# Kernel tuning notes

Hardware: AMD Instinct MI355X
Metric: run time of the kernel (lower is better)

The kernel has to match this reference:

```python
import jax, jax.numpy as jnp
import numpy as np


def setup_inputs() -> dict:
    key = jax.random.key(0)
    k1, k2, k3 = jax.random.split(key, 3)
    B, S, D, H = 16, 4096, 512, 512
    inp = jax.random.normal(k1, (B, S, D), dtype=jnp.float32)
    # torch nn.Linear(D, 3*H): weight (3H, D), bias (3H,)
    W = jax.random.normal(k2, (3 * H, D), dtype=jnp.float32) * (1.0 / np.sqrt(D))
    b = jax.random.normal(k3, (3 * H,), dtype=jnp.float32) * 0.01
    return {"inp": inp, "W": W, "b": b}


def _forget_mult(z, f):
    # z, f: (B, S, H). h_t = f_t*z_t + (1-f_t)*h_{t-1}, h_{-1}=0 (hid=None)
    zt = jnp.swapaxes(z, 0, 1)  # (S, B, H)
    ft = jnp.swapaxes(f, 0, 1)
    h0 = jnp.zeros(z.shape[0:1] + z.shape[2:3], dtype=z.dtype)  # (B, H)

    def step(h, zf):
        zi, fi = zf
        h = fi * zi + (1.0 - fi) * h
        return h, h

    _, hs = jax.lax.scan(step, h0, (zt, ft))
    return jnp.swapaxes(hs, 0, 1)  # (B, S, H)


def reference(inp, W, b):
    # QRNNLayer forward: window=1, output_gate=True, batch_first=True,
    # backward=False, zoneout=0, hid=None.
    y = jnp.einsum('bsd,hd->bsh', inp, W) + b  # (B, S, 3H)
    z_gate, f_gate, o_gate = jnp.split(y, 3, axis=2)
    z_gate = jnp.tanh(z_gate)
    f_gate = jax.nn.sigmoid(f_gate)
    c_gate = _forget_mult(z_gate, f_gate)
    output = jax.nn.sigmoid(o_gate) * c_gate
    return output, c_gate[:, -1]
```

## Files before the change

### kernel.cpp

```cpp
#include <hip/hip_runtime.h>
#include <stdint.h>

#define Bdim 16
#define Sdim 4096
#define Hdim 512
#define Mdim (Bdim*Sdim)
#define N3   (3*Hdim)
#define Kdim 512
#define NCHUNK 128
#define CLEN  (Sdim/NCHUNK)

typedef __bf16 bf16;
typedef __bf16 bf16x4 __attribute__((ext_vector_type(4)));
typedef __bf16 bf16x8 __attribute__((ext_vector_type(8)));
typedef float  f32x4  __attribute__((ext_vector_type(4)));
typedef _Float16 f16;
typedef _Float16 f16x8 __attribute__((ext_vector_type(8)));

__device__ __forceinline__ void gload_lds16(const void* g, void* l) {
  __builtin_amdgcn_global_load_lds(
      (const __attribute__((address_space(1))) uint32_t*)g,
      (__attribute__((address_space(3))) uint32_t*)l, 16, 0, 0);
}

__global__ void __launch_bounds__(256) cvt2_kernel(const float4* __restrict__ a,
                                                   bf16x4* __restrict__ oa, int nA,
                                                   const float4* __restrict__ w,
                                                   bf16x4* __restrict__ ow, int nW) {
  int i = blockIdx.x * blockDim.x + threadIdx.x;
  const float4* src; bf16x4* dst; int j;
  if (i < nA) { src = a; dst = oa; j = i; }
  else { j = i - nA; if (j >= nW) return; src = w; dst = ow; }
  float4 v = src[j];
  bf16x4 o;
  o.x = (bf16)v.x; o.y = (bf16)v.y; o.z = (bf16)v.z; o.w = (bf16)v.w;
  dst[j] = o;
}

#define BM 128
#define BN 256
#define BK2 32
#define NT (Kdim/BK2)
#define LBUF 24576

__global__ void __launch_bounds__(512, 4) gemm_act_kernel(
    const bf16* __restrict__ A, const bf16* __restrict__ Wb,
    const float* __restrict__ bias,
    f16* __restrict__ zbuf, f16* __restrict__ fbuf, f16* __restrict__ ogbuf) {
  __shared__ char lds[2 * LBUF];
  const int tid  = threadIdx.x;
  const int wid  = tid >> 6;
  const int lane = tid & 63;
  const int wr = wid >> 2, wc = wid & 3;
  const int bid = blockIdx.x;
  const int wg  = (bid & 7) * 384 + (bid >> 3);
  const int mt = wg / (N3 / BN);
  const int nt = wg % (N3 / BN);
  const int row0 = mt * BM;

  const bf16* Ag = A  + (size_t)row0 * Kdim;
  const bf16* Bg = Wb + (size_t)(nt * BN) * Kdim;

  uint32_t srcA;
  {
    int row = tid >> 2, slot = tid & 3;
    srcA = (uint32_t)(row * Kdim + ((slot ^ ((row >> 1) & 3)) << 3));
  }
  uint32_t srcB[2];
  #pragma unroll
  for (int i = 0; i < 2; ++i) {
    int c = i * 512 + tid;
    int row = c >> 2, slot = c & 3;
    srcB[i] = (uint32_t)(row * Kdim + ((slot ^ ((row >> 1) & 3)) << 3));
  }
  const uint32_t dstBase = (uint32_t)(wid * 1024);

  uint32_t byteA[4], byteB[4];
  {
    int kslot = lane >> 4;
    #pragma unroll
    for (int m = 0; m < 4; ++m) {
      int row = wr * 64 + m * 16 + (lane & 15);
      byteA[m] = (uint32_t)(row * 64 + ((kslot ^ ((row >> 1) & 3)) << 4));
    }
    #pragma unroll
    for (int n = 0; n < 4; ++n) {
      int row = wc * 64 + n * 16 + (lane & 15);
      byteB[n] = (uint32_t)(8192 + row * 64 + ((kslot ^ ((row >> 1) & 3)) << 4));
    }
  }

  f32x4 acc[4][4];
  #pragma unroll
  for (int m = 0; m < 4; ++m)
    #pragma unroll
    for (int n = 0; n < 4; ++n)
      acc[m][n] = (f32x4){0.f, 0.f, 0.f, 0.f};

  {
    char* Ad = lds; char* Bd = lds + 8192;
    gload_lds16(Ag + srcA, Ad + dstBase);
    #pragma unroll
    for (int i = 0; i < 2; ++i) gload_lds16(Bg + srcB[i], Bd + i * 8192 + dstBase);
  }
  __syncthreads();

  for (int t = 0; t < NT; ++t) {
    if (t + 1 < NT) {
      char* Ad = lds + ((t + 1) & 1) * LBUF; char* Bd = Ad + 8192;
      gload_lds16(Ag + srcA + (t + 1) * BK2, Ad + dstBase);
      #pragma unroll
      for (int i = 0; i < 2; ++i)
        gload_lds16(Bg + srcB[i] + (t + 1) * BK2, Bd + i * 8192 + dstBase);
    }
    const char* Ab = lds + (t & 1) * LBUF;
    bf16x8 af[4], bfrag[4];
    #pragma unroll
    for (int m = 0; m < 4; ++m) af[m] = *(const bf16x8*)(Ab + byteA[m]);
    #pragma unroll
    for (int n = 0; n < 4; ++n) bfrag[n] = *(const bf16x8*)(Ab + byteB[n]);
    #pragma unroll
    for (int m = 0; m < 4; ++m)
      #pragma unroll
      for (int n = 0; n < 4; ++n)
        acc[m][n] = __builtin_amdgcn_mfma_f32_16x16x32_bf16(af[m], bfrag[n], acc[m][n], 0, 0, 0);
    __syncthreads();
  }

  const int gate = nt >> 1;
  const int cbn  = (nt & 1) * 256;
  f16* dst = (gate == 0) ? zbuf : ((gate == 1) ? fbuf : ogbuf);
  float bv[4];
  #pragma unroll
  for (int n = 0; n < 4; ++n)
    bv[n] = bias[gate * Hdim + cbn + wc * 64 + n * 16 + (lane & 15)];

  #pragma unroll
  for (int R = 0; R < 2; ++R) {
    if (wr == R) {
      #pragma unroll
      for (int m = 0; m < 4; ++m) {
        #pragma unroll
        for (int n = 0; n < 4; ++n) {
          int col = wc * 64 + n * 16 + (lane & 15);
          #pragma unroll
          for (int r = 0; r < 4; ++r) {
            int Lrow = m * 16 + (lane >> 4) * 4 + r;
            float y = acc[m][n][r] + bv[n];
            float v;
            if (gate == 0) {
              float e = __expf(2.f * y);
              v = 1.f - 2.f / (e + 1.f);
            } else {
              v = 1.f / (1.f + __expf(-y));
            }
            uint32_t byte = (uint32_t)(Lrow * 512 + col * 2) ^ ((uint32_t)(Lrow & 7) << 4);
            *(f16*)(lds + byte) = (f16)v;
          }
        }
      }
    }
    __syncthreads();
    #pragma unroll
    for (int j = 0; j < 4; ++j) {
      int c = j * 512 + tid;
      int Lrow = c >> 5, col8 = c & 31;
      uint32_t byte = (uint32_t)(Lrow * 512 + col8 * 16) ^ ((uint32_t)(Lrow & 7) << 4);
      f16x8 v = *(const f16x8*)(lds + byte);
      *(f16x8*)&dst[(size_t)(row0 + R * 64 + Lrow) * Hdim + cbn + col8 * 8] = v;
    }
    __syncthreads();
  }
}

__global__ void __launch_bounds__(256) scanA_kernel(const f16x8* __restrict__ z8,
                                                    const f16x8* __restrict__ f8,
                                                    float* __restrict__ Pb,
                                                    float* __restrict__ Qb) {
  int u  = blockIdx.x * blockDim.x + threadIdx.x;
  int ho = u & 63;
  int bc = u >> 6;
  int b  = bc & (Bdim - 1);
  int c  = bc >> 4;
  size_t base = ((size_t)(b * Sdim + c * CLEN)) * 64 + ho;
  float P[8], Q[8];
  #pragma unroll
  for (int j = 0; j < 8; ++j) { P[j] = 1.f; Q[j] = 0.f; }
  #pragma unroll 4
  for (int s = 0; s < CLEN; ++s) {
    f16x8 fv = f8[base], zv = z8[base];
    #pragma unroll
    for (int j = 0; j < 8; ++j) {
      float f = (float)fv[j];
      Q[j] += f * ((float)zv[j] - Q[j]);
      P[j] *= (1.f - f);
    }
    base += 64;
  }
  int outi = ((c * Bdim + b) << 9) + ho * 8;
  *(float4*)&Pb[outi]     = make_float4(P[0], P[1], P[2], P[3]);
  *(float4*)&Pb[outi + 4] = make_float4(P[4], P[5], P[6], P[7]);
  *(float4*)&Qb[outi]     = make_float4(Q[0], Q[1], Q[2], Q[3]);
  *(float4*)&Qb[outi + 4] = make_float4(Q[4], Q[5], Q[6], Q[7]);
}

__global__ void __launch_bounds__(256) scanB_kernel(const float* __restrict__ Pb,
                                                    const float* __restrict__ Qb,
                                                    float* __restrict__ hin,
                                                    float* __restrict__ c_last) {
  int t = blockIdx.x * blockDim.x + threadIdx.x;
  int h = t & (Hdim - 1), b = t >> 9;
  float hs = 0.f;
  #pragma unroll 8
  for (int c = 0; c < NCHUNK; ++c) {
    hin[c * (Bdim * Hdim) + t] = hs;
    int u = ((c * Bdim + b) << 9) + h;
    hs = Pb[u] * hs + Qb[u];
  }
  c_last[t] = hs;
}

__global__ void __launch_bounds__(256) scanC_kernel(const f16x8* __restrict__ z8,
                                                    const f16x8* __restrict__ f8,
                                                    const f16x8* __restrict__ og8,
                                                    const float* __restrict__ hin,
                                                    float4* __restrict__ out4) {
  int u  = blockIdx.x * blockDim.x + threadIdx.x;
  int ho = u & 63;
  int bc = u >> 6;
  int b  = bc & (Bdim - 1);
  int c  = bc >> 4;
  const float* hp = &hin[c * (Bdim * Hdim) + b * Hdim + ho * 8];
  float4 h0 = *(const float4*)hp;
  float4 h1 = *(const float4*)(hp + 4);
  float h[8] = {h0.x, h0.y, h0.z, h0.w, h1.x, h1.y, h1.z, h1.w};
  size_t brow = (size_t)(b * Sdim + c * CLEN);
  size_t base = brow * 64 + ho;
  size_t obase = brow * 128 + ho * 2;
  #pragma unroll 4
  for (int s = 0; s < CLEN; ++s) {
    f16x8 fv = f8[base], zv = z8[base], ov = og8[base];
    #pragma unroll
    for (int j = 0; j < 8; ++j)
      h[j] += (float)fv[j] * ((float)zv[j] - h[j]);
    out4[obase]     = make_float4((float)ov[0] * h[0], (float)ov[1] * h[1],
                                  (float)ov[2] * h[2], (float)ov[3] * h[3]);
    out4[obase + 1] = make_float4((float)ov[4] * h[4], (float)ov[5] * h[5],
                                  (float)ov[6] * h[6], (float)ov[7] * h[7]);
    base += 64;
    obase += 128;
  }
}

extern "C" void kernel_launch(void* const* d_in, const int* in_sizes, int n_in,
                              void* d_out, int out_size, void* d_ws, size_t ws_size,
                              hipStream_t stream) {
  const float* inp  = (const float*)d_in[0];
  const float* W    = (const float*)d_in[1];
  const float* bias = (const float*)d_in[2];
  float* out = (float*)d_out;

  char* ws = (char*)d_ws;
  bf16* Abf = (bf16*)(ws);
  bf16* Wbf = (bf16*)(ws + 67108864);
  f16*  zh  = (f16*) (ws + 68681728);
  f16*  fh  = (f16*) (ws + 135790592);
  f16*  ogh = (f16*) (ws + 202899456);
  float* Pb = (float*)(ws + 270008320);
  float* Qb = (float*)(ws + 274202624);
  float* hin= (float*)(ws + 278396928);

  {
    int nA = (Mdim * Kdim) / 4;
    int nW = (N3 * Kdim) / 4;
    cvt2_kernel<<<(nA + nW + 255) / 256, 256, 0, stream>>>(
        (const float4*)inp, (bf16x4*)Abf, nA, (const float4*)W, (bf16x4*)Wbf, nW);
  }
  gemm_act_kernel<<<(Mdim / BM) * (N3 / BN), 512, 0, stream>>>(Abf, Wbf, bias,
                                                               zh, fh, ogh);
  scanA_kernel<<<(NCHUNK * Bdim * 64) / 256, 256, 0, stream>>>(
      (const f16x8*)zh, (const f16x8*)fh, Pb, Qb);
  scanB_kernel<<<(Bdim * Hdim) / 256, 256, 0, stream>>>(Pb, Qb, hin,
                                                        out + (size_t)Mdim * Hdim);
  scanC_kernel<<<(NCHUNK * Bdim * 64) / 256, 256, 0, stream>>>(
      (const f16x8*)zh, (const f16x8*)fh, (const f16x8*)ogh, hin, (float4*)out);
}
```

Baseline: 299.8 us.

## Fuse fp32-to-bf16 input conversion into GEMM A-tile loading

Removes the separate pass that converted the large activation tensor to bf16. The GEMM now loads fp32 A tiles into registers, converts them to bf16 and writes them to LDS with a two-deep register prefetch. Only the weight is still pre-converted. This saves a full read-and-write pass over the input, but each A tile is now re-read in fp32 by all N-tile blocks, which doubles A traffic inside the GEMM and adds register and VALU pressure.

```diff
diff --git a/kernel.cpp b/kernel.cpp
--- a/kernel.cpp
+++ b/kernel.cpp
@@ -23,18 +23,14 @@
       (__attribute__((address_space(3))) uint32_t*)l, 16, 0, 0);
 }
 
-__global__ void __launch_bounds__(256) cvt2_kernel(const float4* __restrict__ a,
-                                                   bf16x4* __restrict__ oa, int nA,
-                                                   const float4* __restrict__ w,
-                                                   bf16x4* __restrict__ ow, int nW) {
+__global__ void __launch_bounds__(256) cvt_kernel(const float4* __restrict__ in,
+                                                  bf16x4* __restrict__ out, int n4) {
   int i = blockIdx.x * blockDim.x + threadIdx.x;
-  const float4* src; bf16x4* dst; int j;
-  if (i < nA) { src = a; dst = oa; j = i; }
-  else { j = i - nA; if (j >= nW) return; src = w; dst = ow; }
-  float4 v = src[j];
+  if (i >= n4) return;
+  float4 v = in[i];
   bf16x4 o;
   o.x = (bf16)v.x; o.y = (bf16)v.y; o.z = (bf16)v.z; o.w = (bf16)v.w;
-  dst[j] = o;
+  out[i] = o;
 }
 
 #define BM 128
@@ -44,7 +40,7 @@
 #define LBUF 24576
 
 __global__ void __launch_bounds__(512, 4) gemm_act_kernel(
-    const bf16* __restrict__ A, const bf16* __restrict__ Wb,
+    const float* __restrict__ Af, const bf16* __restrict__ Wb,
     const float* __restrict__ bias,
     f16* __restrict__ zbuf, f16* __restrict__ fbuf, f16* __restrict__ ogbuf) {
   __shared__ char lds[2 * LBUF];
@@ -58,13 +54,13 @@
   const int nt = wg % (N3 / BN);
   const int row0 = mt * BM;
 
-  const bf16* Ag = A  + (size_t)row0 * Kdim;
-  const bf16* Bg = Wb + (size_t)(nt * BN) * Kdim;
-
-  uint32_t srcA;
+  const float* Ag = Af + (size_t)row0 * Kdim;
+  const bf16*  Bg = Wb + (size_t)(nt * BN) * Kdim;
+
+  uint32_t srcA32;
   {
     int row = tid >> 2, slot = tid & 3;
-    srcA = (uint32_t)(row * Kdim + ((slot ^ ((row >> 1) & 3)) << 3));
+    srcA32 = (uint32_t)(row * Kdim + ((slot ^ ((row >> 1) & 3)) << 3));
   }
   uint32_t srcB[2];
   #pragma unroll
@@ -97,18 +93,39 @@
     for (int n = 0; n < 4; ++n)
       acc[m][n] = (f32x4){0.f, 0.f, 0.f, 0.f};
 
+  float4 ar[2][2];
+
+  #define LOADA(t_, p_) do {                                                 \
+    const float* Ap = Ag + srcA32 + (t_) * BK2;                              \
+    ar[p_][0] = *(const float4*)(Ap);                                        \
+    ar[p_][1] = *(const float4*)(Ap + 4);                                    \
+  } while (0)
+  #define WRITEA(t_, p_) do {                                                \
+    char* Ad = lds + ((t_) & 1) * LBUF;                                      \
+    bf16x8 fr;                                                               \
+    fr[0] = (bf16)ar[p_][0].x; fr[1] = (bf16)ar[p_][0].y;                    \
+    fr[2] = (bf16)ar[p_][0].z; fr[3] = (bf16)ar[p_][0].w;                    \
+    fr[4] = (bf16)ar[p_][1].x; fr[5] = (bf16)ar[p_][1].y;                    \
+    fr[6] = (bf16)ar[p_][1].z; fr[7] = (bf16)ar[p_][1].w;                    \
+    *(bf16x8*)(Ad + tid * 16) = fr;                                          \
+  } while (0)
+
+  LOADA(0, 0);
+  WRITEA(0, 0);
+  LOADA(1, 1);
   {
-    char* Ad = lds; char* Bd = lds + 8192;
-    gload_lds16(Ag + srcA, Ad + dstBase);
+    char* Bd = lds + 8192;
     #pragma unroll
     for (int i = 0; i < 2; ++i) gload_lds16(Bg + srcB[i], Bd + i * 8192 + dstBase);
   }
   __syncthreads();
 
+  #pragma unroll 2
   for (int t = 0; t < NT; ++t) {
+    if (t + 1 < NT) WRITEA(t + 1, (t + 1) & 1);
+    if (t + 2 < NT) LOADA(t + 2, t & 1);
     if (t + 1 < NT) {
-      char* Ad = lds + ((t + 1) & 1) * LBUF; char* Bd = Ad + 8192;
-      gload_lds16(Ag + srcA + (t + 1) * BK2, Ad + dstBase);
+      char* Bd = lds + ((t + 1) & 1) * LBUF + 8192;
       #pragma unroll
       for (int i = 0; i < 2; ++i)
         gload_lds16(Bg + srcB[i] + (t + 1) * BK2, Bd + i * 8192 + dstBase);
@@ -261,7 +278,6 @@
   float* out = (float*)d_out;
 
   char* ws = (char*)d_ws;
-  bf16* Abf = (bf16*)(ws);
   bf16* Wbf = (bf16*)(ws + 67108864);
   f16*  zh  = (f16*) (ws + 68681728);
   f16*  fh  = (f16*) (ws + 135790592);
@@ -271,12 +287,10 @@
   float* hin= (float*)(ws + 278396928);
 
   {
-    int nA = (Mdim * Kdim) / 4;
-    int nW = (N3 * Kdim) / 4;
-    cvt2_kernel<<<(nA + nW + 255) / 256, 256, 0, stream>>>(
-        (const float4*)inp, (bf16x4*)Abf, nA, (const float4*)W, (bf16x4*)Wbf, nW);
-  }
-  gemm_act_kernel<<<(Mdim / BM) * (N3 / BN), 512, 0, stream>>>(Abf, Wbf, bias,
+    int n4 = (N3 * Kdim) / 4;
+    cvt_kernel<<<(n4 + 255) / 256, 256, 0, stream>>>((const float4*)W, (bf16x4*)Wbf, n4);
+  }
+  gemm_act_kernel<<<(Mdim / BM) * (N3 / BN), 512, 0, stream>>>(inp, Wbf, bias,
                                                                zh, fh, ogh);
   scanA_kernel<<<(NCHUNK * Bdim * 64) / 256, 256, 0, stream>>>(
       (const f16x8*)zh, (const f16x8*)fh, Pb, Qb);
```

Result: slower. 325.8 us (+8.7%).
